# Performance work log

Hardware: AMD Instinct MI355X
Metric: run time of the kernel (lower is better)

The kernel has to match this reference:

```python
import jax, jax.numpy as jnp
import numpy as np

B = 16384
F_IN = 768
F_OUT = 512

def setup_inputs() -> dict:
    key = jax.random.key(0)
    k1, k2, k3, k4, k5, k6 = jax.random.split(key, 6)
    # densified sparse multi-hot boards (post to_dense())
    stm = jax.random.uniform(k1, (B, F_IN), dtype=jnp.float32)
    nstm = jax.random.uniform(k2, (B, F_IN), dtype=jnp.float32)
    s1 = 1.0 / np.sqrt(F_IN)
    s2 = 1.0 / np.sqrt(2 * F_OUT)
    W1 = jax.random.normal(k3, (F_OUT, F_IN), dtype=jnp.float32) * s1
    b1 = jax.random.normal(k4, (F_OUT,), dtype=jnp.float32) * s1
    W2 = jax.random.normal(k5, (1, 2 * F_OUT), dtype=jnp.float32) * s2
    b2 = jax.random.normal(k6, (1,), dtype=jnp.float32) * s2
    return {"stm": stm, "nstm": nstm, "W1": W1, "b1": b1, "W2": W2, "b2": b2}

def reference(stm, nstm, W1, b1, W2, b2):
    # shared feature transformer applied to both perspectives
    stm_p = stm @ W1.T + b1    # [B, F_OUT]
    nstm_p = nstm @ W1.T + b1  # [B, F_OUT]
    hidden = jnp.clip(jnp.concatenate((stm_p, nstm_p), axis=1), 0.0, 1.0)  # [B, 2*F_OUT]
    return jax.nn.sigmoid(hidden @ W2.T + b2)  # [B, 1]
```

## Files before the change

kernel.cpp:

```cpp
#include <hip/hip_runtime.h>
#include <hip/hip_bf16.h>

#define BATCH 16384
#define FIN   768
#define FOUT  512

#define BK 32
#define NT (FIN / BK)

typedef __attribute__((ext_vector_type(8))) short short8;
typedef __attribute__((ext_vector_type(4))) float floatx4;

__device__ __forceinline__ unsigned int cvt_pk_bf16(float a, float b) {
    unsigned int r;
    asm("v_cvt_pk_bf16_f32 %0, %1, %2" : "=v"(r) : "v"(a), "v"(b));
    return r;
}

__device__ __forceinline__ void load_lds_16(const void* g, void* l) {
    __builtin_amdgcn_global_load_lds(
        (const __attribute__((address_space(1))) unsigned int*)g,
        (__attribute__((address_space(3))) unsigned int*)l,
        16, 0, 0);
}

__global__ __launch_bounds__(256) void cvt_w1(
    const float* __restrict__ W1, unsigned short* __restrict__ W1b)
{
    int base = (blockIdx.x * 256 + threadIdx.x) * 8;
    float4 a = *(const float4*)(W1 + base);
    float4 b = *(const float4*)(W1 + base + 4);
    uint4 o;
    o.x = cvt_pk_bf16(a.x, a.y); o.y = cvt_pk_bf16(a.z, a.w);
    o.z = cvt_pk_bf16(b.x, b.y); o.w = cvt_pk_bf16(b.z, b.w);
    *(uint4*)(W1b + base) = o;
}

__global__ __launch_bounds__(1024, 4) void pn_gemm(
    const float* __restrict__ stm, const float* __restrict__ nstm,
    const unsigned short* __restrict__ W1b, const float* __restrict__ b1,
    const float* __restrict__ W2, const float* __restrict__ b2,
    float* __restrict__ out)
{
    __shared__ __align__(16) unsigned short As[2][128 * 32];
    __shared__ __align__(16) unsigned short Bs[2][512 * 32];

    const int tid  = threadIdx.x;
    const int lane = tid & 63;
    const int wave = tid >> 6;
    const int wrow = wave >> 3;
    const int wcol = wave & 7;
    const int quad = lane >> 4;
    const int l16  = lane & 15;
    const int l3   = l16 & 3;

    const int b0 = blockIdx.x * 64;

    const int arow = tid >> 2;
    const int ach  = tid & 3;
    const float* aSrc = nullptr;
    if (wave < 8)
        aSrc = ((arow < 64) ? stm  + (size_t)(b0 + arow) * FIN
                            : nstm + (size_t)(b0 + arow - 64) * FIN) + ach * 8;
    const int aOff = arow * 32 + (ach ^ (arow & 3)) * 8;

    const int brow = lane >> 2;
    const int bch  = (lane & 3) ^ (brow & 3);

    floatx4 acc[4][4];
    #pragma unroll
    for (int i = 0; i < 4; ++i)
        #pragma unroll
        for (int j = 0; j < 4; ++j)
            acc[i][j] = (floatx4)0.0f;

    float4 ap0, ap1;
    if (wave < 8) {
        ap0 = *(const float4*)(aSrc);
        ap1 = *(const float4*)(aSrc + 4);
    }
    #pragma unroll
    for (int i = 0; i < 2; ++i) {
        const int J = wave * 2 + i;
        load_lds_16(W1b + (size_t)(J * 16 + brow) * FIN + bch * 8,
                    &Bs[0][J * 16 * 32]);
    }

    for (int t = 0; t < NT; ++t) {
        const int cur = t & 1;
        const int nxt = cur ^ 1;

        if (wave < 8) {
            uint4 o;
            o.x = cvt_pk_bf16(ap0.x, ap0.y); o.y = cvt_pk_bf16(ap0.z, ap0.w);
            o.z = cvt_pk_bf16(ap1.x, ap1.y); o.w = cvt_pk_bf16(ap1.z, ap1.w);
            *(uint4*)(&As[cur][aOff]) = o;
        }
        __syncthreads();

        if (t + 1 < NT) {
            const int kn = (t + 1) * BK;
            #pragma unroll
            for (int i = 0; i < 2; ++i) {
                const int J = wave * 2 + i;
                load_lds_16(W1b + (size_t)(J * 16 + brow) * FIN + kn + bch * 8,
                            &Bs[nxt][J * 16 * 32]);
            }
            if (wave < 8) {
                ap0 = *(const float4*)(aSrc + kn);
                ap1 = *(const float4*)(aSrc + kn + 4);
            }
        }

        short8 af[4], bfr[4];
        #pragma unroll
        for (int mi = 0; mi < 4; ++mi) {
            const int m = wrow * 64 + mi * 16 + l16;
            af[mi] = *(const short8*)(&As[cur][m * 32 + ((quad ^ l3) * 8)]);
        }
        #pragma unroll
        for (int ni = 0; ni < 4; ++ni) {
            const int n = wcol * 64 + ni * 16 + l16;
            bfr[ni] = *(const short8*)(&Bs[cur][n * 32 + ((quad ^ l3) * 8)]);
        }
        #pragma unroll
        for (int mi = 0; mi < 4; ++mi)
            #pragma unroll
            for (int ni = 0; ni < 4; ++ni)
                acc[mi][ni] = __builtin_amdgcn_mfma_f32_16x16x32_bf16(
                    af[mi], bfr[ni], acc[mi][ni], 0, 0, 0);
    }

    float b1v[4], w2v[4];
    #pragma unroll
    for (int ni = 0; ni < 4; ++ni) {
        int col = wcol * 64 + ni * 16 + l16;
        b1v[ni] = b1[col];
        w2v[ni] = W2[wrow * FOUT + col];
    }

    __syncthreads();
    float* Epi = (float*)As;

    #pragma unroll
    for (int mi = 0; mi < 4; ++mi) {
        #pragma unroll
        for (int r = 0; r < 4; ++r) {
            float s = 0.0f;
            #pragma unroll
            for (int ni = 0; ni < 4; ++ni) {
                float h = acc[mi][ni][r] + b1v[ni];
                h = fminf(fmaxf(h, 0.0f), 1.0f);
                s += h * w2v[ni];
            }
            s += __shfl_xor(s, 1);
            s += __shfl_xor(s, 2);
            s += __shfl_xor(s, 4);
            s += __shfl_xor(s, 8);
            if (l16 == 0) {
                Epi[(wrow * 64 + mi * 16 + quad * 4 + r) * 8 + wcol] = s;
            }
        }
    }
    __syncthreads();

    if (tid < 64) {
        float x = b2[0];
        #pragma unroll
        for (int j = 0; j < 8; ++j)
            x += Epi[tid * 8 + j] + Epi[(tid + 64) * 8 + j];
        out[b0 + tid] = 1.0f / (1.0f + expf(-x));
    }
}

extern "C" void kernel_launch(void* const* d_in, const int* in_sizes, int n_in,
                              void* d_out, int out_size, void* d_ws, size_t ws_size,
                              hipStream_t stream)
{
    (void)in_sizes; (void)n_in; (void)out_size; (void)ws_size;
    const float* stm  = (const float*)d_in[0];
    const float* nstm = (const float*)d_in[1];
    const float* W1   = (const float*)d_in[2];
    const float* b1   = (const float*)d_in[3];
    const float* W2   = (const float*)d_in[4];
    const float* b2   = (const float*)d_in[5];
    float* out = (float*)d_out;
    unsigned short* W1b = (unsigned short*)d_ws;

    cvt_w1<<<dim3((FOUT * FIN) / (256 * 8)), dim3(256), 0, stream>>>(W1, W1b);
    pn_gemm<<<dim3(BATCH / 64), dim3(1024), 0, stream>>>(
        stm, nstm, W1b, b1, W2, b2, out);
}
```

Baseline: 148.7 us.

## Use 8 waves with 128x64 per-wave tiles and new LDS swizzle

Drops the block from 16 waves to 8. Each wave now covers all 128 A rows (stm and nstm) against its own 64 output columns, and all threads take part in loading A. This doubles the per-wave MFMA work per B fragment loaded, cutting LDS fragment reads per MFMA, and removes the idle loader waves. The LDS layouts for A and B get a new rotation-based swizzle meant to avoid bank conflicts. In exchange, accumulator registers double to 128 floats per lane, which lowers occupancy.

```diff
diff --git a/kernel.cpp b/kernel.cpp
--- a/kernel.cpp
+++ b/kernel.cpp
@@ -36,7 +36,7 @@
     *(uint4*)(W1b + base) = o;
 }
 
-__global__ __launch_bounds__(1024, 4) void pn_gemm(
+__global__ __launch_bounds__(512, 2) void pn_gemm(
     const float* __restrict__ stm, const float* __restrict__ nstm,
     const unsigned short* __restrict__ W1b, const float* __restrict__ b1,
     const float* __restrict__ W2, const float* __restrict__ b2,
@@ -48,49 +48,42 @@
     const int tid  = threadIdx.x;
     const int lane = tid & 63;
     const int wave = tid >> 6;
-    const int wrow = wave >> 3;
-    const int wcol = wave & 7;
     const int quad = lane >> 4;
     const int l16  = lane & 15;
-    const int l3   = l16 & 3;
 
     const int b0 = blockIdx.x * 64;
 
     const int arow = tid >> 2;
     const int ach  = tid & 3;
-    const float* aSrc = nullptr;
-    if (wave < 8)
-        aSrc = ((arow < 64) ? stm  + (size_t)(b0 + arow) * FIN
-                            : nstm + (size_t)(b0 + arow - 64) * FIN) + ach * 8;
-    const int aOff = arow * 32 + (ach ^ (arow & 3)) * 8;
+    const float* aSrc = ((arow < 64) ? stm  + (size_t)(b0 + arow) * FIN
+                                     : nstm + (size_t)(b0 + arow - 64) * FIN) + ach * 8;
+    const int aSlot = (((arow & 15) + 4 * ach) & 15) + 16 * ach;
+    const int aOff  = (arow >> 4) * 512 + aSlot * 8;
 
-    const int brow = lane >> 2;
-    const int bch  = (lane & 3) ^ (brow & 3);
+    const int brig = lane & 15;
+    const int bch  = ((lane >> 4) - brig) & 3;
 
-    floatx4 acc[4][4];
+    floatx4 acc[8][4];
     #pragma unroll
-    for (int i = 0; i < 4; ++i)
+    for (int i = 0; i < 8; ++i)
         #pragma unroll
         for (int j = 0; j < 4; ++j)
             acc[i][j] = (floatx4)0.0f;
 
-    float4 ap0, ap1;
-    if (wave < 8) {
-        ap0 = *(const float4*)(aSrc);
-        ap1 = *(const float4*)(aSrc + 4);
-    }
+    float4 ap0 = *(const float4*)(aSrc);
+    float4 ap1 = *(const float4*)(aSrc + 4);
     #pragma unroll
-    for (int i = 0; i < 2; ++i) {
-        const int J = wave * 2 + i;
-        load_lds_16(W1b + (size_t)(J * 16 + brow) * FIN + bch * 8,
-                    &Bs[0][J * 16 * 32]);
+    for (int i = 0; i < 4; ++i) {
+        const int J = wave * 4 + i;
+        load_lds_16(W1b + (size_t)(J * 16 + brig) * FIN + bch * 8,
+                    &Bs[0][J * 512]);
     }
 
     for (int t = 0; t < NT; ++t) {
         const int cur = t & 1;
         const int nxt = cur ^ 1;
 
-        if (wave < 8) {
+        {
             uint4 o;
             o.x = cvt_pk_bf16(ap0.x, ap0.y); o.y = cvt_pk_bf16(ap0.z, ap0.w);
             o.z = cvt_pk_bf16(ap1.x, ap1.y); o.w = cvt_pk_bf16(ap1.z, ap1.w);
@@ -101,49 +94,50 @@
         if (t + 1 < NT) {
             const int kn = (t + 1) * BK;
             #pragma unroll
-            for (int i = 0; i < 2; ++i) {
-                const int J = wave * 2 + i;
-                load_lds_16(W1b + (size_t)(J * 16 + brow) * FIN + kn + bch * 8,
-                            &Bs[nxt][J * 16 * 32]);
+            for (int i = 0; i < 4; ++i) {
+                const int J = wave * 4 + i;
+                load_lds_16(W1b + (size_t)(J * 16 + brig) * FIN + kn + bch * 8,
+                            &Bs[nxt][J * 512]);
             }
-            if (wave < 8) {
-                ap0 = *(const float4*)(aSrc + kn);
-                ap1 = *(const float4*)(aSrc + kn + 4);
-            }
+            ap0 = *(const float4*)(aSrc + kn);
+            ap1 = *(const float4*)(aSrc + kn + 4);
         }
 
-        short8 af[4], bfr[4];
+        short8 af[8], bfr[4];
         #pragma unroll
-        for (int mi = 0; mi < 4; ++mi) {
-            const int m = wrow * 64 + mi * 16 + l16;
-            af[mi] = *(const short8*)(&As[cur][m * 32 + ((quad ^ l3) * 8)]);
+        for (int mi = 0; mi < 8; ++mi) {
+            const int slot = ((l16 + 4 * quad) & 15) + 16 * quad;
+            af[mi] = *(const short8*)(&As[cur][mi * 512 + slot * 8]);
         }
         #pragma unroll
         for (int ni = 0; ni < 4; ++ni) {
-            const int n = wcol * 64 + ni * 16 + l16;
-            bfr[ni] = *(const short8*)(&Bs[cur][n * 32 + ((quad ^ l3) * 8)]);
+            const int G = wave * 4 + ni;
+            const int slot = l16 + 16 * ((quad + l16) & 3);
+            bfr[ni] = *(const short8*)(&Bs[cur][G * 512 + slot * 8]);
         }
         #pragma unroll
-        for (int mi = 0; mi < 4; ++mi)
+        for (int mi = 0; mi < 8; ++mi)
             #pragma unroll
             for (int ni = 0; ni < 4; ++ni)
                 acc[mi][ni] = __builtin_amdgcn_mfma_f32_16x16x32_bf16(
                     af[mi], bfr[ni], acc[mi][ni], 0, 0, 0);
     }
 
-    float b1v[4], w2v[4];
+    float b1v[4], w2v0[4], w2v1[4];
     #pragma unroll
     for (int ni = 0; ni < 4; ++ni) {
-        int col = wcol * 64 + ni * 16 + l16;
-        b1v[ni] = b1[col];
-        w2v[ni] = W2[wrow * FOUT + col];
+        int col = wave * 64 + ni * 16 + l16;
+        b1v[ni]  = b1[col];
+        w2v0[ni] = W2[col];
+        w2v1[ni] = W2[FOUT + col];
     }
 
     __syncthreads();
     float* Epi = (float*)As;
 
     #pragma unroll
-    for (int mi = 0; mi < 4; ++mi) {
+    for (int mi = 0; mi < 8; ++mi) {
+        const float* w2v = (mi < 4) ? w2v0 : w2v1;
         #pragma unroll
         for (int r = 0; r < 4; ++r) {
             float s = 0.0f;
@@ -158,7 +152,7 @@
             s += __shfl_xor(s, 4);
             s += __shfl_xor(s, 8);
             if (l16 == 0) {
-                Epi[(wrow * 64 + mi * 16 + quad * 4 + r) * 8 + wcol] = s;
+                Epi[(mi * 16 + quad * 4 + r) * 8 + wave] = s;
             }
         }
     }
@@ -188,6 +182,6 @@
     unsigned short* W1b = (unsigned short*)d_ws;
 
     cvt_w1<<<dim3((FOUT * FIN) / (256 * 8)), dim3(256), 0, stream>>>(W1, W1b);
-    pn_gemm<<<dim3(BATCH / 64), dim3(1024), 0, stream>>>(
+    pn_gemm<<<dim3(BATCH / 64), dim3(512), 0, stream>>>(
         stm, nstm, W1b, b1, W2, b2, out);
 }
```

Result: slower. 152.8 us (+2.8%).
